# Performance work log

Measured on AMD Instinct MI355X. Metric: run time of the kernel, lower is better.

The kernel has to match this reference:

```python
import jax, jax.numpy as jnp
import numpy as np

EPS = 1e-8

def setup_inputs() -> dict:
    key = jax.random.key(0)
    k1, k2 = jax.random.split(key)
    B, IN, OUT, G = 32768, 256, 256, 5
    x = jax.random.normal(k1, (B, IN), dtype=jnp.float32)
    grid = jnp.linspace(-1.0, 1.0, G).astype(jnp.float32)
    coef = jax.random.normal(k2, (OUT, IN, G), dtype=jnp.float32) * 0.1
    scale = jnp.ones((OUT, IN), dtype=jnp.float32)
    bias = jnp.zeros((OUT,), dtype=jnp.float32)
    return {"x": x, "grid": grid, "coef": coef, "scale": scale, "bias": bias}

def reference(x, grid, coef, scale, bias):
    # global min-max normalization to [-1, 1]
    xmin, xmax = x.min(), x.max()
    xn = 2.0 * (x - xmin) / (xmax - xmin + EPS) - 1.0
    # cubic bump B-spline-like basis: (batch, in, grid)
    dist = jnp.abs(xn[..., None] - grid)
    basis = jnp.where(dist < 1.0, 1.0 - dist ** 3, 0.0)
    basis = basis / (basis.sum(axis=-1, keepdims=True) + EPS)
    # fused contraction over (in, grid); equals ((basis*coef).sum(-1)*scale).sum(-1)
    w = coef * scale[..., None]          # (out, in, grid)
    out = jnp.einsum('big,oig->bo', basis, w) + bias
    return out
```

## Files before the change

kernel.cpp:

```cpp
#include <hip/hip_runtime.h>
#include <stdint.h>


#define B_SZ   32768
#define IN_SZ  256
#define OUT_SZ 256
#define EPSF   1e-8f
#define NMB    2048

typedef __bf16 bf16x8 __attribute__((ext_vector_type(8)));
typedef unsigned short ushort8 __attribute__((ext_vector_type(8)));
typedef float floatx16 __attribute__((ext_vector_type(16)));

union frag_u { uint4 u; bf16x8 v; };

__device__ __forceinline__ unsigned short f2bf(float f) {
  unsigned u = __float_as_uint(f);
  u += 0x7FFFu + ((u >> 16) & 1u);
  return (unsigned short)(u >> 16);
}


__global__ void __launch_bounds__(256) prep_kernel(const float* __restrict__ coef,
                                                   const float* __restrict__ scale,
                                                   const float* __restrict__ x,
                                                   unsigned short* __restrict__ wf,
                                                   float* __restrict__ part, int n4) {
  const int t = threadIdx.x;
  if (blockIdx.x < 256) {
    int idx = blockIdx.x * 256 + t;
    int o = idx >> 8, i = idx & 255;
    float s = scale[idx];
    const float* c = coef + (size_t)idx * 5;
    ushort8 v;
    v[0] = f2bf(c[0] * s); v[1] = f2bf(c[1] * s); v[2] = f2bf(c[2] * s);
    v[3] = f2bf(c[3] * s); v[4] = f2bf(c[4] * s);
    v[5] = 0; v[6] = 0; v[7] = 0;
    int chunk = (((o >> 5) * 64 + (i >> 2)) * 2 + ((i >> 1) & 1)) * 64
                + (i & 1) * 32 + (o & 31);
    *(ushort8*)(wf + (size_t)chunk * 8) = v;
  } else {
    int mb = blockIdx.x - 256;
    const float4* x4 = (const float4*)x;
    int i = mb * 256 + t;
    float lmin = 1e30f, lmax = -1e30f;
    #pragma unroll
    for (int k = 0; k < 4; ++k) {
      float4 v = x4[i + k * (NMB * 256)];
      lmin = fminf(lmin, fminf(fminf(v.x, v.y), fminf(v.z, v.w)));
      lmax = fmaxf(lmax, fmaxf(fmaxf(v.x, v.y), fmaxf(v.z, v.w)));
    }
    #pragma unroll
    for (int off = 32; off >= 1; off >>= 1) {
      lmin = fminf(lmin, __shfl_down(lmin, off, 64));
      lmax = fmaxf(lmax, __shfl_down(lmax, off, 64));
    }
    __shared__ float smn[4], smx[4];
    if ((t & 63) == 0) { smn[t >> 6] = lmin; smx[t >> 6] = lmax; }
    __syncthreads();
    if (t == 0) {
      part[2 * mb]     = fminf(fminf(smn[0], smn[1]), fminf(smn[2], smn[3]));
      part[2 * mb + 1] = fmaxf(fmaxf(smx[0], smx[1]), fmaxf(smx[2], smx[3]));
    }
  }
}

__device__ __forceinline__ bf16x8 basisfrag(float xval, float scA, float scB) {
  float xn = fmaf(xval, scA, scB);
  float d0 = xn + 1.0f, d1 = xn + 0.5f, d3 = xn - 0.5f, d4 = xn - 1.0f;
  float b0 = fmaxf(fmaf(d0 * d0, -fabsf(d0), 1.0f), 0.0f);
  float b1 = fmaxf(fmaf(d1 * d1, -fabsf(d1), 1.0f), 0.0f);
  float b2 = fmaxf(fmaf(xn * xn, -fabsf(xn), 1.0f), 0.0f);
  float b3 = fmaxf(fmaf(d3 * d3, -fabsf(d3), 1.0f), 0.0f);
  float b4 = fmaxf(fmaf(d4 * d4, -fabsf(d4), 1.0f), 0.0f);
  float sum = ((b0 + b1) + (b2 + b3)) + b4;
  float inv = __builtin_amdgcn_rcpf(sum);
  b0 *= inv; b1 *= inv; b2 *= inv; b3 *= inv; b4 *= inv;
  frag_u r;
  r.u.x = __builtin_amdgcn_perm(__float_as_uint(b1), __float_as_uint(b0), 0x07060302u);
  r.u.y = __builtin_amdgcn_perm(__float_as_uint(b3), __float_as_uint(b2), 0x07060302u);
  r.u.z = __float_as_uint(b4) >> 16;
  r.u.w = 0u;
  return r.v;
}

__global__ void __launch_bounds__(256, 2) kan_gemm(
    const float* __restrict__ x,
    const unsigned short* __restrict__ wf,
    const float* __restrict__ bias,
    const float* __restrict__ part,
    float* __restrict__ out)
{
  __shared__ __align__(16) unsigned short Bb[2][16384];
  __shared__ float2 red[4];

  const int t = threadIdx.x;
  const int lane = t & 63;
  const int wm = t >> 6;
  const int l31 = lane & 31, lh = lane >> 5;
  const int by = blockIdx.x & 1;
  const int bx = blockIdx.x >> 1;
  const int bRow = bx * 128;
  const int bCol = by * 128;
  const int row = bRow + wm * 32 + l31;

  auto stage = [&](int c, int buf) {
    #pragma unroll
    for (int r = 0; r < 8; ++r) {
      int idx = r * 4 + wm;
      const unsigned short* src = wf +
          ((size_t)(((by * 4 + (idx >> 3)) * 64 + (c * 4 + ((idx >> 1) & 3))) * 2
                    + (idx & 1))) * 512 + (size_t)lane * 8;
      __builtin_amdgcn_global_load_lds(
          (const __attribute__((address_space(1))) unsigned int*)src,
          (__attribute__((address_space(3))) unsigned int*)(&Bb[buf][idx * 512 + lane * 8]),
          16, 0, 0);
    }
  };

  const float* xrow = x + (size_t)row * IN_SZ;

  stage(0, 0);
  float4 xq[4], xqn[4];
  #pragma unroll
  for (int g = 0; g < 4; ++g) xq[g] = *(const float4*)(xrow + g * 4);

  float mn = 1e30f, mx = -1e30f;
  const float2* part2 = (const float2*)part;
  #pragma unroll
  for (int k = 0; k < NMB / 256; ++k) {
    float2 p = part2[k * 256 + t];
    mn = fminf(mn, p.x); mx = fmaxf(mx, p.y);
  }
  #pragma unroll
  for (int off = 32; off >= 1; off >>= 1) {
    mn = fminf(mn, __shfl_down(mn, off, 64));
    mx = fmaxf(mx, __shfl_down(mx, off, 64));
  }
  if (lane == 0) red[wm] = make_float2(mn, mx);
  __syncthreads();
  mn = fminf(fminf(red[0].x, red[1].x), fminf(red[2].x, red[3].x));
  mx = fmaxf(fmaxf(red[0].y, red[1].y), fmaxf(red[2].y, red[3].y));
  const float scA = 2.0f / (mx - mn + EPSF);
  const float scB = -mn * scA - 1.0f;

  floatx16 acc[4] = {};
  bf16x8 br[2][8];

  auto ldsB = [&](int ktr, int buf, bf16x8* dst) {
    #pragma unroll
    for (int q = 0; q < 8; ++q) {
      int ni = q >> 1, ks = q & 1;
      dst[q] = *(const bf16x8*)(&Bb[buf][((ni * 4 + ktr) * 2 + ks) * 512 + lane * 8]);
    }
  };

  for (int c = 0; c < 16; ++c) {
    const int buf = c & 1;

    __syncthreads();

    if (c < 15) {
      stage(c + 1, buf ^ 1);
      #pragma unroll
      for (int g = 0; g < 4; ++g)
        xqn[g] = *(const float4*)(xrow + (c + 1) * 16 + g * 4);
    }

    ldsB(0, buf, br[0]);

    bf16x8 af0[4], af1[4];
    #pragma unroll
    for (int ktr = 0; ktr < 4; ++ktr) {
      af0[ktr] = basisfrag(lh ? xq[ktr].y : xq[ktr].x, scA, scB);
      af1[ktr] = basisfrag(lh ? xq[ktr].w : xq[ktr].z, scA, scB);
    }

    #pragma unroll
    for (int ktr = 0; ktr < 4; ++ktr) {
      if (ktr < 3) ldsB(ktr + 1, buf, br[(ktr + 1) & 1]);
      bf16x8* B = br[ktr & 1];
      #pragma unroll
      for (int ni = 0; ni < 4; ++ni)
        acc[ni] = __builtin_amdgcn_mfma_f32_32x32x16_bf16(af0[ktr], B[ni * 2 + 0], acc[ni], 0, 0, 0);
      #pragma unroll
      for (int ni = 0; ni < 4; ++ni)
        acc[ni] = __builtin_amdgcn_mfma_f32_32x32x16_bf16(af1[ktr], B[ni * 2 + 1], acc[ni], 0, 0, 0);
    }

    if (c < 15) {
      #pragma unroll
      for (int g = 0; g < 4; ++g) xq[g] = xqn[g];
    }
  }

  #pragma unroll
  for (int ni = 0; ni < 4; ++ni) {
    int o = bCol + ni * 32 + l31;
    float bs = bias[o];
    int rb = bRow + wm * 32 + 4 * lh;
    #pragma unroll
    for (int reg = 0; reg < 16; ++reg) {
      int r = rb + (reg & 3) + 8 * (reg >> 2);
      out[(size_t)r * OUT_SZ + o] = acc[ni][reg] + bs;
    }
  }
}

extern "C" void kernel_launch(void* const* d_in, const int* in_sizes, int n_in,
                              void* d_out, int out_size, void* d_ws, size_t ws_size,
                              hipStream_t stream) {
  const float* x     = (const float*)d_in[0];
  const float* coef  = (const float*)d_in[2];
  const float* scale = (const float*)d_in[3];
  const float* bias  = (const float*)d_in[4];
  float* out = (float*)d_out;

  size_t need = 16384 + (size_t)OUT_SZ * IN_SZ * 8 * 2;
  if (ws_size < need) return;

  float* part = (float*)d_ws;
  unsigned short* wf = (unsigned short*)((char*)d_ws + 16384);

  prep_kernel<<<256 + NMB, 256, 0, stream>>>(coef, scale, x, wf, part,
                                             (B_SZ * IN_SZ) / 4);
  kan_gemm<<<512, 256, 0, stream>>>(x, wf, bias, part, out);
}
```

Baseline: 132.4 us.

## Pack five basis values densely along K to drop zero-padded MFMA lanes

```diff
diff --git a/kernel.cpp b/kernel.cpp
--- a/kernel.cpp
+++ b/kernel.cpp
@@ -13,6 +13,10 @@
 typedef float floatx16 __attribute__((ext_vector_type(16)));
 
 union frag_u { uint4 u; bf16x8 v; };
+
+#define PKHH 0x07060302u
+#define PKLL 0x05040100u
+#define PKHL 0x05040302u
 
 __device__ __forceinline__ unsigned short f2bf(float f) {
   unsigned u = __float_as_uint(f);
@@ -27,20 +31,23 @@
                                                    unsigned short* __restrict__ wf,
                                                    float* __restrict__ part, int n4) {
   const int t = threadIdx.x;
-  if (blockIdx.x < 256) {
-    int idx = blockIdx.x * 256 + t;
-    int o = idx >> 8, i = idx & 255;
-    float s = scale[idx];
-    const float* c = coef + (size_t)idx * 5;
+  if (blockIdx.x < 160) {
+    int b = blockIdx.x;
+    int c = b / 10, r = b - c * 10;
+    int kt = r >> 1, lh = r & 1;
+    int o = t;
+    const float* cp = coef + (size_t)o * 1280 + c * 80 + lh * 40 + kt * 8;
+    const float* sp = scale + o * 256 + c * 16 + lh * 8;
     ushort8 v;
-    v[0] = f2bf(c[0] * s); v[1] = f2bf(c[1] * s); v[2] = f2bf(c[2] * s);
-    v[3] = f2bf(c[3] * s); v[4] = f2bf(c[4] * s);
-    v[5] = 0; v[6] = 0; v[7] = 0;
-    int chunk = (((o >> 5) * 64 + (i >> 2)) * 2 + ((i >> 1) & 1)) * 64
-                + (i & 1) * 32 + (o & 31);
-    *(ushort8*)(wf + (size_t)chunk * 8) = v;
+    #pragma unroll
+    for (int j = 0; j < 8; ++j) {
+      int il = (kt * 8 + j) / 5;
+      v[j] = f2bf(cp[j] * sp[il]);
+    }
+    int seg = (c * 8 + (o >> 5)) * 5 + kt;
+    *(ushort8*)(wf + (size_t)seg * 512 + (lh * 32 + (o & 31)) * 8) = v;
   } else {
-    int mb = blockIdx.x - 256;
+    int mb = blockIdx.x - 160;
     const float4* x4 = (const float4*)x;
     int i = mb * 256 + t;
     float lmin = 1e30f, lmax = -1e30f;
@@ -65,7 +72,9 @@
   }
 }
 
-__device__ __forceinline__ bf16x8 basisfrag(float xval, float scA, float scB) {
+struct quint { unsigned u0, u1, u2; };
+
+__device__ __forceinline__ quint quintet(float xval, float scA, float scB) {
   float xn = fmaf(xval, scA, scB);
   float d0 = xn + 1.0f, d1 = xn + 0.5f, d3 = xn - 0.5f, d4 = xn - 1.0f;
   float b0 = fmaxf(fmaf(d0 * d0, -fabsf(d0), 1.0f), 0.0f);
@@ -76,12 +85,11 @@
   float sum = ((b0 + b1) + (b2 + b3)) + b4;
   float inv = __builtin_amdgcn_rcpf(sum);
   b0 *= inv; b1 *= inv; b2 *= inv; b3 *= inv; b4 *= inv;
-  frag_u r;
-  r.u.x = __builtin_amdgcn_perm(__float_as_uint(b1), __float_as_uint(b0), 0x07060302u);
-  r.u.y = __builtin_amdgcn_perm(__float_as_uint(b3), __float_as_uint(b2), 0x07060302u);
-  r.u.z = __float_as_uint(b4) >> 16;
-  r.u.w = 0u;
-  return r.v;
+  quint q;
+  q.u0 = __builtin_amdgcn_perm(__float_as_uint(b1), __float_as_uint(b0), PKHH);
+  q.u1 = __builtin_amdgcn_perm(__float_as_uint(b3), __float_as_uint(b2), PKHH);
+  q.u2 = __float_as_uint(b4) >> 16;
+  return q;
 }
 
 __global__ void __launch_bounds__(256, 2) kan_gemm(
@@ -91,29 +99,25 @@
     const float* __restrict__ part,
     float* __restrict__ out)
 {
-  __shared__ __align__(16) unsigned short Bb[2][16384];
+  __shared__ __align__(16) unsigned short Bb[2][10240];
   __shared__ float2 red[4];
 
   const int t = threadIdx.x;
   const int lane = t & 63;
   const int wm = t >> 6;
   const int l31 = lane & 31, lh = lane >> 5;
-  const int by = blockIdx.x & 1;
-  const int bx = blockIdx.x >> 1;
-  const int bRow = bx * 128;
-  const int bCol = by * 128;
+  const int bRow = blockIdx.x * 128;
+  const int bCol = blockIdx.y * 128;
   const int row = bRow + wm * 32 + l31;
 
   auto stage = [&](int c, int buf) {
     #pragma unroll
-    for (int r = 0; r < 8; ++r) {
-      int idx = r * 4 + wm;
+    for (int r = 0; r < 5; ++r) {
       const unsigned short* src = wf +
-          ((size_t)(((by * 4 + (idx >> 3)) * 64 + (c * 4 + ((idx >> 1) & 3))) * 2
-                    + (idx & 1))) * 512 + (size_t)lane * 8;
+          ((size_t)((c * 8 + blockIdx.y * 4 + wm) * 5 + r)) * 512 + (size_t)lane * 8;
       __builtin_amdgcn_global_load_lds(
           (const __attribute__((address_space(1))) unsigned int*)src,
-          (__attribute__((address_space(3))) unsigned int*)(&Bb[buf][idx * 512 + lane * 8]),
+          (__attribute__((address_space(3))) unsigned int*)(&Bb[buf][(r * 4 + wm) * 512 + lane * 8]),
           16, 0, 0);
     }
   };
@@ -145,14 +149,12 @@
   const float scB = -mn * scA - 1.0f;
 
   floatx16 acc[4] = {};
-  bf16x8 br[2][8];
-
-  auto ldsB = [&](int ktr, int buf, bf16x8* dst) {
-    #pragma unroll
-    for (int q = 0; q < 8; ++q) {
-      int ni = q >> 1, ks = q & 1;
-      dst[q] = *(const bf16x8*)(&Bb[buf][((ni * 4 + ktr) * 2 + ks) * 512 + lane * 8]);
-    }
+  bf16x8 br[2][4];
+
+  auto ldsB = [&](int kt, int buf, bf16x8* dst) {
+    #pragma unroll
+    for (int q = 0; q < 4; ++q)
+      dst[q] = *(const bf16x8*)(&Bb[buf][(kt * 4 + q) * 512 + lane * 8]);
   };
 
   for (int c = 0; c < 16; ++c) {
@@ -169,24 +171,61 @@
 
     ldsB(0, buf, br[0]);
 
-    bf16x8 af0[4], af1[4];
-    #pragma unroll
-    for (int ktr = 0; ktr < 4; ++ktr) {
-      af0[ktr] = basisfrag(lh ? xq[ktr].y : xq[ktr].x, scA, scB);
-      af1[ktr] = basisfrag(lh ? xq[ktr].w : xq[ktr].z, scA, scB);
-    }
-
-    #pragma unroll
-    for (int ktr = 0; ktr < 4; ++ktr) {
-      if (ktr < 3) ldsB(ktr + 1, buf, br[(ktr + 1) & 1]);
-      bf16x8* B = br[ktr & 1];
-      #pragma unroll
-      for (int ni = 0; ni < 4; ++ni)
-        acc[ni] = __builtin_amdgcn_mfma_f32_32x32x16_bf16(af0[ktr], B[ni * 2 + 0], acc[ni], 0, 0, 0);
-      #pragma unroll
-      for (int ni = 0; ni < 4; ++ni)
-        acc[ni] = __builtin_amdgcn_mfma_f32_32x32x16_bf16(af1[ktr], B[ni * 2 + 1], acc[ni], 0, 0, 0);
-    }
+    float4 xa = lh ? xq[2] : xq[0];
+    float4 xb = lh ? xq[3] : xq[1];
+    quint q0 = quintet(xa.x, scA, scB), q1 = quintet(xa.y, scA, scB);
+    quint q2 = quintet(xa.z, scA, scB), q3 = quintet(xa.w, scA, scB);
+    quint q4 = quintet(xb.x, scA, scB), q5 = quintet(xb.y, scA, scB);
+    quint q6 = quintet(xb.z, scA, scB), q7 = quintet(xb.w, scA, scB);
+
+    frag_u a;
+    bf16x8* B;
+
+    ldsB(1, buf, br[1]);
+    a.u.x = q0.u0; a.u.y = q0.u1;
+    a.u.z = __builtin_amdgcn_perm(q1.u0, q0.u2, PKLL);
+    a.u.w = __builtin_amdgcn_perm(q1.u1, q1.u0, PKHL);
+    B = br[0];
+    #pragma unroll
+    for (int ni = 0; ni < 4; ++ni)
+      acc[ni] = __builtin_amdgcn_mfma_f32_32x32x16_bf16(a.v, B[ni], acc[ni], 0, 0, 0);
+
+    ldsB(2, buf, br[0]);
+    a.u.x = __builtin_amdgcn_perm(q1.u2, q1.u1, PKHL);
+    a.u.y = q2.u0; a.u.z = q2.u1;
+    a.u.w = __builtin_amdgcn_perm(q3.u0, q2.u2, PKLL);
+    B = br[1];
+    #pragma unroll
+    for (int ni = 0; ni < 4; ++ni)
+      acc[ni] = __builtin_amdgcn_mfma_f32_32x32x16_bf16(a.v, B[ni], acc[ni], 0, 0, 0);
+
+    ldsB(3, buf, br[1]);
+    a.u.x = __builtin_amdgcn_perm(q3.u1, q3.u0, PKHL);
+    a.u.y = __builtin_amdgcn_perm(q3.u2, q3.u1, PKHL);
+    a.u.z = q4.u0; a.u.w = q4.u1;
+    B = br[0];
+    #pragma unroll
+    for (int ni = 0; ni < 4; ++ni)
+      acc[ni] = __builtin_amdgcn_mfma_f32_32x32x16_bf16(a.v, B[ni], acc[ni], 0, 0, 0);
+
+    ldsB(4, buf, br[0]);
+    a.u.x = __builtin_amdgcn_perm(q5.u0, q4.u2, PKLL);
+    a.u.y = __builtin_amdgcn_perm(q5.u1, q5.u0, PKHL);
+    a.u.z = __builtin_amdgcn_perm(q5.u2, q5.u1, PKHL);
+    a.u.w = q6.u0;
+    B = br[1];
+    #pragma unroll
+    for (int ni = 0; ni < 4; ++ni)
+      acc[ni] = __builtin_amdgcn_mfma_f32_32x32x16_bf16(a.v, B[ni], acc[ni], 0, 0, 0);
+
+    a.u.x = q6.u1;
+    a.u.y = __builtin_amdgcn_perm(q7.u0, q6.u2, PKLL);
+    a.u.z = __builtin_amdgcn_perm(q7.u1, q7.u0, PKHL);
+    a.u.w = __builtin_amdgcn_perm(q7.u2, q7.u1, PKHL);
+    B = br[0];
+    #pragma unroll
+    for (int ni = 0; ni < 4; ++ni)
+      acc[ni] = __builtin_amdgcn_mfma_f32_32x32x16_bf16(a.v, B[ni], acc[ni], 0, 0, 0);
 
     if (c < 15) {
       #pragma unroll
@@ -216,13 +255,14 @@
   const float* bias  = (const float*)d_in[4];
   float* out = (float*)d_out;
 
-  size_t need = 16384 + (size_t)OUT_SZ * IN_SZ * 8 * 2;
+  size_t need = 16384 + (size_t)640 * 1024;
   if (ws_size < need) return;
 
   float* part = (float*)d_ws;
   unsigned short* wf = (unsigned short*)((char*)d_ws + 16384);
 
-  prep_kernel<<<256 + NMB, 256, 0, stream>>>(coef, scale, x, wf, part,
+  prep_kernel<<<160 + NMB, 256, 0, stream>>>(coef, scale, x, wf, part,
                                              (B_SZ * IN_SZ) / 4);
-  kan_gemm<<<512, 256, 0, stream>>>(x, wf, bias, part, out);
-}
+  dim3 g(B_SZ / 128, OUT_SZ / 128);
+  kan_gemm<<<g, 256, 0, stream>>>(x, wf, bias, part, out);
+}
```

After: 123.4 us. 1.07x faster.
